# Kernel optimization log

Hardware: AMD Instinct MI355X
Metric: run time of the kernel (lower is better)

## Reference

```python
import jax, jax.numpy as jnp
import numpy as np

N = 1_000_000
LIMS = ((0.0, 51.2), (-25.6, 25.6), (-2.0, 4.4))
SIZES = (256, 256, 32)
GM = np.array([0.2, 0.2, 0.2], np.float32)      # grid_meters
MINS = np.array([0.0, -25.6, -2.0], np.float32)  # xmin, ymin, zmin
OFFSET = 0.5
INIT = 32  # init_size; VFE units = INIT // 2 = 16


def setup_inputs() -> dict:
    key = jax.random.key(0)
    ks = jax.random.split(key, 20)
    lo = jnp.array([l[0] for l in LIMS], jnp.float32)
    hi = jnp.array([l[1] for l in LIMS], jnp.float32)
    # keep points strictly inside lims so quantized idx stays in range
    u = jax.random.uniform(ks[0], (N, 3), minval=1e-3, maxval=1.0 - 1e-3)
    xyz = lo + (hi - lo) * u
    inten = jax.random.uniform(ks[1], (N, 1))
    pc = jnp.concatenate([xyz, inten], axis=1).astype(jnp.float32)
    indicator = jnp.array([0, N // 2, N], jnp.int32)

    def lin(k, o, i):
        return (0.02 * jax.random.normal(k, (o, i), jnp.float32))

    def bias(k, o):
        return (0.02 * jax.random.normal(k, (o,), jnp.float32))

    U = INIT // 2  # 16, VFE units (last_vfe=False)
    return dict(
        pc=pc, indicator=indicator,
        w05=lin(ks[2], U, 10), b05=bias(ks[3], U),
        ww05=lin(ks[4], U, 6), wb05=bias(ks[5], U),
        w1=lin(ks[6], U, 10), b1=bias(ks[7], U),
        ww1=lin(ks[8], U, 6), wb1=bias(ks[9], U),
        am_w=lin(ks[10], INIT, 6), am_b=bias(ks[11], INIT),
        at_w=lin(ks[12], INIT, 2 * INIT), at_b=bias(ks[13], INIT),
        af_w=lin(ks[14], INIT, INIT), af_b=bias(ks[15], INIT),
    )


def _unique_inverse(ids):
    # emulate torch.unique(dim=0, return_inverse=True) via sort+rank on linear voxel ids
    n = ids.shape[0]
    order = jnp.argsort(ids)
    s = ids[order]
    new = jnp.concatenate([jnp.zeros((1,), jnp.int32), (s[1:] != s[:-1]).astype(jnp.int32)])
    ranks = jnp.cumsum(new)
    return jnp.zeros((n,), jnp.int32).at[order].set(ranks)


def _voxel_coords(pc, indicator, scale):
    n = pc.shape[0]
    B = indicator.shape[0] - 1
    bt = jnp.repeat(jnp.arange(B, dtype=jnp.int32), jnp.diff(indicator), total_repeat_length=n)
    nx = int(SIZES[0] // scale); ny = int(SIZES[1] // scale); nz = int(SIZES[2] // scale)
    def quant(col, lim, size):
        idx = (col - lim[0]) / (lim[1] - lim[0]) * float(size)
        return idx.astype(jnp.int32)
    xi = quant(pc[:, 0], LIMS[0], nx)
    yi = quant(pc[:, 1], LIMS[1], ny)
    zi = quant(pc[:, 2], LIMS[2], nz)
    coords = jnp.stack([bt, xi, yi, zi], axis=-1)  # [n,4] bxyz_indx
    lid = ((bt * nx + xi) * ny + yi) * nz + zi     # lexicographic-consistent linear id
    return coords, lid


def _scale_features(pc, coords, inv, Wl, bl, Ww, bw):
    # add_pcmean_and_gridmean + VFELayerMinus (activate=False, gs=None)
    n = pc.shape[0]
    cnt = jax.ops.segment_sum(jnp.ones((n,), jnp.float32), inv, num_segments=n)
    pc_mean = jax.ops.segment_sum(pc[:, :3], inv, num_segments=n) / jnp.maximum(cnt, 1.0)[:, None]
    mm = pc[:, :3] - pc_mean[inv]                                   # pc_mean_minus
    gm = jnp.asarray(GM); mins = jnp.asarray(MINS)
    gmm = pc[:, :3] - ((coords[:, 1:].astype(jnp.float32) + OFFSET) * gm + mins)  # pc_gridmean_minus
    feat = jnp.concatenate([pc, mm, gmm], axis=1)   # [n,10]
    mean = jnp.concatenate([mm, gmm], axis=1)       # [n,6]
    x = feat @ Wl.T + bl                            # [n,16]
    x = x * (mean @ Ww.T + bw)
    mx = jax.ops.segment_max(x, inv, num_segments=n)
    return jnp.concatenate([x, mx[inv]], axis=1), mean  # [n,32], [n,6]


def reference(pc, indicator, w05, b05, ww05, wb05, w1, b1, ww1, wb1,
              am_w, am_b, at_w, at_b, af_w, af_b):
    n = pc.shape[0]
    coords05, lid05 = _voxel_coords(pc, indicator, 0.5)
    coords1, lid1 = _voxel_coords(pc, indicator, 1)
    inv05 = _unique_inverse(lid05)
    inv1 = _unique_inverse(lid1)
    f05, _ = _scale_features(pc, coords05, inv05, w05, b05, ww05, wb05)
    f1, mean1 = _scale_features(pc, coords1, inv1, w1, b1, ww1, wb1)
    agg = jax.nn.relu(mean1 @ am_w.T + am_b) * \
          jax.nn.relu(jnp.concatenate([f05, f1], axis=1) @ at_w.T + at_b)
    agg = agg @ af_w.T + af_b                       # [n,32]
    maxf = jax.ops.segment_max(agg, inv1, num_segments=n)
    cnt = jax.ops.segment_sum(jnp.ones((n,), jnp.float32), inv1, num_segments=n)
    maxf = jnp.where(cnt[:, None] > 0, maxf, 0.0)   # pad empty rows (torch output has no such rows)
    coord_ind = jnp.zeros((n, 4), jnp.int32).at[inv1].set(coords1)  # unique coords, padded to n
    return maxf, coord_ind, inv1
```

## Files before the change

kernel.cpp:

```cpp
#include <hip/hip_runtime.h>
#include <cstdint>
#include <cstdio>


struct Coords { int xi, yi, zi; };

__device__ __forceinline__ Coords quantc(float x, float y, float z, float sx, float sy, float sz) {
    Coords c;
    c.xi = (int)(((x - 0.0f)  / 51.2f) * sx);
    c.yi = (int)(((y + 25.6f) / 51.2f) * sy);
    c.zi = (int)(((z + 2.0f)  / 6.4f)  * sz);
    return c;
}

__device__ __forceinline__ int batch_of(int i, const int* __restrict__ ind, int B) {
    int bt = 0;
    for (int b = 1; b < B; ++b) if (i >= ind[b]) bt = b;
    return bt;
}

__device__ __forceinline__ unsigned f2o(float f) {
    unsigned u = __float_as_uint(f);
    return (u & 0x80000000u) ? ~u : (u | 0x80000000u);
}
__device__ __forceinline__ float o2f(unsigned u) {
    return (u & 0x80000000u) ? __uint_as_float(u ^ 0x80000000u) : __uint_as_float(~u);
}
#define NEG_O 0x007FFFFFu

__device__ __forceinline__ unsigned short f2bf(float x) {
    unsigned u = __float_as_uint(x);
    unsigned r = (u + 0x7FFFu + ((u >> 16) & 1u)) >> 16;
    return (unsigned short)r;
}
__device__ __forceinline__ float bf2f(unsigned h) {
    return __uint_as_float(h << 16);
}

__device__ __forceinline__ void compute_x16(
    float px, float py, float pz, float pw,
    float mx_, float my_, float mz_, Coords c,
    const float* __restrict__ W, const float* __restrict__ Bv,
    const float* __restrict__ Ww, const float* __restrict__ Wb,
    float* __restrict__ x, float* __restrict__ mean6) {
    float gx = px - (((float)c.xi + 0.5f) * 0.2f + 0.0f);
    float gy = py - (((float)c.yi + 0.5f) * 0.2f + (-25.6f));
    float gz = pz - (((float)c.zi + 0.5f) * 0.2f + (-2.0f));
    float mmx = px - mx_, mmy = py - my_, mmz = pz - mz_;
    float feat[10] = {px, py, pz, pw, mmx, mmy, mmz, gx, gy, gz};
    float mean[6]  = {mmx, mmy, mmz, gx, gy, gz};
#pragma unroll
    for (int j = 0; j < 6; ++j) mean6[j] = mean[j];
#pragma unroll
    for (int o = 0; o < 16; ++o) {
        float a = Bv[o];
#pragma unroll
        for (int j = 0; j < 10; ++j) a += feat[j] * W[o * 10 + j];
        float g = Wb[o];
#pragma unroll
        for (int j = 0; j < 6; ++j) g += mean[j] * Ww[o * 6 + j];
        x[o] = a * g;
    }
}


__global__ __launch_bounds__(256) void k_bits(
    const float4* __restrict__ pc, const int* __restrict__ ind, int B, int n,
    unsigned* __restrict__ mask05, unsigned* __restrict__ mask1) {
    int i = blockIdx.x * 256 + threadIdx.x;
    if (i >= n) return;
    float4 p = pc[i];
    int bt = batch_of(i, ind, B);
    Coords c05 = quantc(p.x, p.y, p.z, 512.f, 512.f, 64.f);
    Coords c1  = quantc(p.x, p.y, p.z, 256.f, 256.f, 32.f);
    int lid05 = ((bt * 512 + c05.xi) * 512 + c05.yi) * 64 + c05.zi;
    int lid1  = ((bt * 256 + c1.xi)  * 256 + c1.yi)  * 32 + c1.zi;
    atomicOr(&mask05[lid05 >> 5], 1u << (lid05 & 31));
    atomicOr(&mask1[lid1 >> 5],  1u << (lid1 & 31));
}

__global__ __launch_bounds__(256) void k_chunk2(
    const unsigned* __restrict__ maskA, unsigned* __restrict__ bsumA, int nWA, int nBA,
    const unsigned* __restrict__ maskB, unsigned* __restrict__ bsumB, int nWB) {
    const unsigned* mask; unsigned* bsum; int nW, blk;
    if ((int)blockIdx.x < nBA) { mask = maskA; bsum = bsumA; nW = nWA; blk = blockIdx.x; }
    else { mask = maskB; bsum = bsumB; nW = nWB; blk = blockIdx.x - nBA; }
    int t = threadIdx.x;
    int base = blk * 2048 + t;
    unsigned tot = 0;
#pragma unroll
    for (int k = 0; k < 8; ++k) {
        int w = base + k * 256;
        if (w < nW) tot += __popc(mask[w]);
    }
    __shared__ unsigned s[256];
    s[t] = tot;
    __syncthreads();
    for (int off = 128; off > 0; off >>= 1) {
        if (t < off) s[t] += s[t + off];
        __syncthreads();
    }
    if (t == 0) bsum[blk] = s[0];
}

__global__ __launch_bounds__(256) void k_chunku2(
    const unsigned* __restrict__ cntA, unsigned* __restrict__ bsumA,
    const unsigned* __restrict__ cntB, unsigned* __restrict__ bsumB,
    int nElem, int nCh) {
    const unsigned* val; unsigned* bsum; int blk;
    if ((int)blockIdx.x < nCh) { val = cntA; bsum = bsumA; blk = blockIdx.x; }
    else { val = cntB; bsum = bsumB; blk = blockIdx.x - nCh; }
    int t = threadIdx.x;
    int base = blk * 2048 + t;
    unsigned tot = 0;
#pragma unroll
    for (int k = 0; k < 8; ++k) {
        int w = base + k * 256;
        if (w < nElem) tot += val[w];
    }
    __shared__ unsigned s[256];
    s[t] = tot;
    __syncthreads();
    for (int off = 128; off > 0; off >>= 1) {
        if (t < off) s[t] += s[t + off];
        __syncthreads();
    }
    if (t == 0) bsum[blk] = s[0];
}

__global__ __launch_bounds__(1024) void k_scan2(
    const unsigned* __restrict__ bsumA, unsigned* __restrict__ bprefA,
    unsigned* __restrict__ UoutA, int nA,
    const unsigned* __restrict__ bsumB, unsigned* __restrict__ bprefB,
    unsigned* __restrict__ UoutB, int nB) {
    const unsigned* bsum; unsigned* bpref; unsigned* Uout; int nBn;
    if (blockIdx.x == 0) { bsum = bsumA; bpref = bprefA; Uout = UoutA; nBn = nA; }
    else { bsum = bsumB; bpref = bprefB; Uout = UoutB; nBn = nB; }
    __shared__ unsigned s[1024];
    int t = threadIdx.x;
    int ipt = (nBn + 1023) >> 10;
    unsigned tot = 0;
    for (int k = 0; k < ipt; ++k) {
        int e = t * ipt + k;
        if (e < nBn) tot += bsum[e];
    }
    s[t] = tot;
    __syncthreads();
    for (int off = 1; off < 1024; off <<= 1) {
        unsigned v = 0;
        if (t >= off) v = s[t - off];
        __syncthreads();
        if (t >= off) s[t] += v;
        __syncthreads();
    }
    unsigned run = s[t] - tot;
    for (int k = 0; k < ipt; ++k) {
        int e = t * ipt + k;
        if (e < nBn) { bpref[e] = run; run += bsum[e]; }
    }
    if (t == 1023 && Uout) *Uout = s[1023];
}

__global__ __launch_bounds__(256) void k_wpref2(
    const unsigned* __restrict__ maskA, const unsigned* __restrict__ bprefA,
    unsigned* __restrict__ wprefA, int nWA, int nBA,
    const unsigned* __restrict__ maskB, const unsigned* __restrict__ bprefB,
    unsigned* __restrict__ wprefB, int nWB) {
    const unsigned* mask; const unsigned* bpref; unsigned* wpref; int nW, blk;
    if ((int)blockIdx.x < nBA) { mask = maskA; bpref = bprefA; wpref = wprefA; nW = nWA; blk = blockIdx.x; }
    else { mask = maskB; bpref = bprefB; wpref = wprefB; nW = nWB; blk = blockIdx.x - nBA; }
    int t = threadIdx.x;
    int base = blk * 2048 + t * 8;
    unsigned p[8];
    unsigned tot = 0;
#pragma unroll
    for (int k = 0; k < 8; ++k) {
        int w = base + k;
        p[k] = (w < nW) ? __popc(mask[w]) : 0u;
        tot += p[k];
    }
    __shared__ unsigned s[256];
    s[t] = tot;
    __syncthreads();
    for (int off = 1; off < 256; off <<= 1) {
        unsigned v = 0;
        if (t >= off) v = s[t - off];
        __syncthreads();
        if (t >= off) s[t] += v;
        __syncthreads();
    }
    unsigned run = bpref[blk] + (s[t] - tot);
#pragma unroll
    for (int k = 0; k < 8; ++k) {
        int w = base + k;
        if (w < nW) { wpref[w] = run; run += p[k]; }
    }
}

__global__ __launch_bounds__(256) void k_eprefu2(
    const unsigned* __restrict__ cntA, const unsigned* __restrict__ bprefA,
    unsigned* __restrict__ startA,
    const unsigned* __restrict__ cntB, const unsigned* __restrict__ bprefB,
    unsigned* __restrict__ startB,
    int nElem, int nCh) {
    const unsigned* val; const unsigned* bpref; unsigned* epref; int blk;
    if ((int)blockIdx.x < nCh) { val = cntA; bpref = bprefA; epref = startA; blk = blockIdx.x; }
    else { val = cntB; bpref = bprefB; epref = startB; blk = blockIdx.x - nCh; }
    int t = threadIdx.x;
    int base = blk * 2048 + t * 8;
    unsigned p[8];
    unsigned tot = 0;
#pragma unroll
    for (int k = 0; k < 8; ++k) {
        int w = base + k;
        p[k] = (w < nElem) ? val[w] : 0u;
        tot += p[k];
    }
    __shared__ unsigned s[256];
    s[t] = tot;
    __syncthreads();
    for (int off = 1; off < 256; off <<= 1) {
        unsigned v = 0;
        if (t >= off) v = s[t - off];
        __syncthreads();
        if (t >= off) s[t] += v;
        __syncthreads();
    }
    unsigned run = bpref[blk] + (s[t] - tot);
#pragma unroll
    for (int k = 0; k < 8; ++k) {
        int w = base + k;
        if (w < nElem) { epref[w] = run; run += p[k]; }
    }
}


__global__ __launch_bounds__(256) void k_rank(
    const float4* __restrict__ pc, const int* __restrict__ ind, int B, int n,
    const unsigned* __restrict__ mask05, const unsigned* __restrict__ wp05,
    const unsigned* __restrict__ mask1, const unsigned* __restrict__ wp1,
    unsigned* __restrict__ inv05, unsigned* __restrict__ inv1,
    unsigned* __restrict__ cnt05, unsigned* __restrict__ cnt1,
    unsigned* __restrict__ slot05, unsigned* __restrict__ slot1,
    float* __restrict__ outCoord, float* __restrict__ outInv) {
    int i = blockIdx.x * 256 + threadIdx.x;
    if (i >= n) return;
    float4 p = pc[i];
    int bt = batch_of(i, ind, B);
    Coords c05 = quantc(p.x, p.y, p.z, 512.f, 512.f, 64.f);
    Coords c1  = quantc(p.x, p.y, p.z, 256.f, 256.f, 32.f);
    int lid05 = ((bt * 512 + c05.xi) * 512 + c05.yi) * 64 + c05.zi;
    int lid1  = ((bt * 256 + c1.xi)  * 256 + c1.yi)  * 32 + c1.zi;

    unsigned w = (unsigned)lid05 >> 5, b = (unsigned)lid05 & 31u;
    unsigned r05 = wp05[w] + __popc(mask05[w] & ((1u << b) - 1u));
    w = (unsigned)lid1 >> 5; b = (unsigned)lid1 & 31u;
    unsigned r1 = wp1[w] + __popc(mask1[w] & ((1u << b) - 1u));

    inv05[i] = r05;
    inv1[i] = r1;
    outInv[i] = (float)r1;
    ((float4*)outCoord)[r1] = make_float4((float)bt, (float)c1.xi, (float)c1.yi, (float)c1.zi);

    slot05[i] = atomicAdd(&cnt05[r05], 1u);
    slot1[i]  = atomicAdd(&cnt1[r1], 1u);
}

__global__ __launch_bounds__(256) void k_slot(
    const unsigned* __restrict__ inv05, const unsigned* __restrict__ inv1,
    const unsigned* __restrict__ slot05, const unsigned* __restrict__ slot1,
    const unsigned* __restrict__ start05, const unsigned* __restrict__ start1,
    unsigned* __restrict__ rec05 , unsigned* __restrict__ rec1 , int n) {
    int i = blockIdx.x * 256 + threadIdx.x;
    if (i >= n) return;
    unsigned r05 = inv05[i], r1 = inv1[i];
    unsigned p05 = start05[r05] + slot05[i];
    unsigned p1  = start1[r1] + slot1[i];
    ((uint2*)rec05)[p05] = make_uint2((unsigned)i, r05);
    ((uint4*)rec1)[p1]   = make_uint4((unsigned)i, r1, r05, 0u);
}

__global__ __launch_bounds__(256) void k_segmean2(
    const float4* __restrict__ pc,
    const unsigned* __restrict__ rec05, const unsigned* __restrict__ start05,
    const unsigned* __restrict__ cnt05, float4* __restrict__ mean05,
    const unsigned* __restrict__ rec1, const unsigned* __restrict__ start1,
    const unsigned* __restrict__ cnt1, float4* __restrict__ mean1,
    unsigned char* __restrict__ flags, unsigned* __restrict__ outMaxU,
    int n, int gpts) {
    if ((int)blockIdx.x >= 2 * gpts) {
        int blk3 = blockIdx.x - 2 * gpts;
        int b = blk3 * 256 + threadIdx.x + 1;
        if (b >= gpts) return;
        int j = b * 256;
        if (j >= n) return;
        unsigned r = rec1[(size_t)j * 4 + 1];
        if (start1[r] < (unsigned)j) {
            flags[r] = 1;
            unsigned* row = outMaxU + (size_t)r * 32;
#pragma unroll
            for (int o = 0; o < 32; ++o) row[o] = NEG_O;
        }
        return;
    }
    const unsigned* rec; const unsigned* start; const unsigned* cnt;
    float4* meanOut; int stride, blk;
    if ((int)blockIdx.x < gpts) {
        rec = rec05; start = start05; cnt = cnt05; meanOut = mean05; stride = 2; blk = blockIdx.x;
    } else {
        rec = rec1; start = start1; cnt = cnt1; meanOut = mean1; stride = 4; blk = blockIdx.x - gpts;
    }
    int j = blk * 256 + threadIdx.x;
    int lane = threadIdx.x & 63;
    bool live = j < n;
    unsigned r = 0xFFFFFFFFu;
    float sx = 0.f, sy = 0.f, sz = 0.f;
    if (live) {
        unsigned pi = rec[(size_t)j * stride];
        r = rec[(size_t)j * stride + 1];
        float4 p = pc[pi];
        sx = p.x; sy = p.y; sz = p.z;
    }
#pragma unroll
    for (int d = 1; d < 64; d <<= 1) {
        unsigned rn = (unsigned)__shfl_down((int)r, d);
        float ax = __shfl_down(sx, d);
        float ay = __shfl_down(sy, d);
        float az = __shfl_down(sz, d);
        bool ok = (lane + d) < 64 && rn == r;
        if (ok) { sx += ax; sy += ay; sz += az; }
    }
    if (!live) return;
    if (j != (int)start[r]) return;
    unsigned c = cnt[r];
    unsigned end = j + c;
    unsigned waveEnd = ((unsigned)j & ~63u) + 64u;
    for (unsigned j2 = waveEnd; j2 < end; ++j2) {
        float4 q = pc[rec[(size_t)j2 * stride]];
        sx += q.x; sy += q.y; sz += q.z;
    }
    float cf = (float)c;
    meanOut[r] = make_float4(sx / cf, sy / cf, sz / cf, 0.f);
}

__global__ __launch_bounds__(256) void k_segmx2(
    const float4* __restrict__ pc,
    const unsigned* __restrict__ rec05, const unsigned* __restrict__ start05,
    const unsigned* __restrict__ cnt05, const float4* __restrict__ mean05,
    const float* __restrict__ w05, const float* __restrict__ b05,
    const float* __restrict__ ww05, const float* __restrict__ wb05,
    unsigned short* __restrict__ mx05,
    const unsigned* __restrict__ rec1, const unsigned* __restrict__ start1,
    const unsigned* __restrict__ cnt1, const float4* __restrict__ mean1,
    const float* __restrict__ w1, const float* __restrict__ b1,
    const float* __restrict__ ww1, const float* __restrict__ wb1,
    unsigned short* __restrict__ mx1,
    int n, int gpts) {
    const unsigned* rec; const unsigned* start; const unsigned* cnt;
    const float4* meanIn; const float* W; const float* Bv; const float* Ww;
    const float* Wb; unsigned short* mxOut; int stride, blk;
    float sx_, sy_, sz_;
    if ((int)blockIdx.x < gpts) {
        rec = rec05; start = start05; cnt = cnt05; meanIn = mean05;
        W = w05; Bv = b05; Ww = ww05; Wb = wb05; mxOut = mx05; stride = 2;
        sx_ = 512.f; sy_ = 512.f; sz_ = 64.f; blk = blockIdx.x;
    } else {
        rec = rec1; start = start1; cnt = cnt1; meanIn = mean1;
        W = w1; Bv = b1; Ww = ww1; Wb = wb1; mxOut = mx1; stride = 4;
        sx_ = 256.f; sy_ = 256.f; sz_ = 32.f; blk = blockIdx.x - gpts;
    }
    __shared__ float buf[256][17];
    int t = threadIdx.x;
    int j = blk * 256 + t;
    bool live = j < n;
    unsigned r = 0;
    float x[16], d6[6];
    if (live) {
        unsigned pi = rec[(size_t)j * stride];
        r = rec[(size_t)j * stride + 1];
        float4 p = pc[pi];
        float4 mv = meanIn[r];
        Coords cc = quantc(p.x, p.y, p.z, sx_, sy_, sz_);
        compute_x16(p.x, p.y, p.z, p.w, mv.x, mv.y, mv.z, cc, W, Bv, Ww, Wb, x, d6);
    } else {
#pragma unroll
        for (int o = 0; o < 16; ++o) x[o] = 0.f;
    }
#pragma unroll
    for (int o = 0; o < 16; ++o) buf[t][o] = x[o];
    __syncthreads();
    if (!live || j != (int)start[r]) return;
    unsigned c = cnt[r];
    unsigned end = j + c;
    unsigned blockEnd = ((unsigned)blk + 1u) * 256u;
    unsigned inEnd = end < blockEnd ? end : blockEnd;
    for (unsigned j2 = j + 1; j2 < inEnd; ++j2) {
        int t2 = t + (int)(j2 - (unsigned)j);
#pragma unroll
        for (int o = 0; o < 16; ++o) x[o] = fmaxf(x[o], buf[t2][o]);
    }
    float4 mv = meanIn[r];
    for (unsigned j2 = blockEnd; j2 < end; ++j2) {
        float4 q = pc[rec[(size_t)j2 * stride]];
        Coords cc = quantc(q.x, q.y, q.z, sx_, sy_, sz_);
        float x2[16];
        compute_x16(q.x, q.y, q.z, q.w, mv.x, mv.y, mv.z, cc, W, Bv, Ww, Wb, x2, d6);
#pragma unroll
        for (int o = 0; o < 16; ++o) x[o] = fmaxf(x[o], x2[o]);
    }
    unsigned pk[8];
#pragma unroll
    for (int k = 0; k < 8; ++k)
        pk[k] = (unsigned)f2bf(x[2 * k]) | ((unsigned)f2bf(x[2 * k + 1]) << 16);
    uint4* mr = (uint4*)(mxOut + (size_t)r * 16);
    mr[0] = make_uint4(pk[0], pk[1], pk[2], pk[3]);
    mr[1] = make_uint4(pk[4], pk[5], pk[6], pk[7]);
}

__global__ __launch_bounds__(256, 3) void k_val(
    const float4* __restrict__ pc,
    const unsigned* __restrict__ rec1,
    const unsigned* __restrict__ start1, const unsigned* __restrict__ cnt1,
    const float4* __restrict__ mean05, const unsigned short* __restrict__ mx05,
    const float4* __restrict__ mean1, const unsigned short* __restrict__ mx1,
    const float* __restrict__ w05, const float* __restrict__ b05,
    const float* __restrict__ ww05, const float* __restrict__ wb05,
    const float* __restrict__ w1g, const float* __restrict__ b1g,
    const float* __restrict__ ww1, const float* __restrict__ wb1,
    const float* __restrict__ am_w, const float* __restrict__ am_b,
    const float* __restrict__ at_w, const float* __restrict__ at_b,
    const float* __restrict__ af_w, const float* __restrict__ af_b,
    float* __restrict__ outMax, int n) {
    __shared__ float buf[256][17];
    int t = threadIdx.x;
    int j = blockIdx.x * 256 + t;
    bool live = j < n;
    unsigned r = 0, s = 0, c = 0;
    bool bound = false;
    float at[32];
    if (live) {
        uint4 rc = ((const uint4*)rec1)[j];
        float4 p = pc[rc.x];
        r = rc.y;
        unsigned r05 = rc.z;
        s = start1[r];
        c = cnt1[r];
        bound = (s >> 8) != ((s + c - 1) >> 8);

#pragma unroll
        for (int o = 0; o < 32; ++o) at[o] = at_b[o];

        {
            const uint4* m4 = (const uint4*)(mx1 + (size_t)r * 16);
            uint4 a = m4[0], b2 = m4[1];
            unsigned pw[8] = {a.x, a.y, a.z, a.w, b2.x, b2.y, b2.z, b2.w};
#pragma unroll
            for (int k = 0; k < 8; ++k) {
                float e0 = bf2f(pw[k] & 0xFFFFu);
                float e1 = bf2f(pw[k] >> 16);
#pragma unroll
                for (int o = 0; o < 32; ++o)
                    at[o] += e0 * at_w[o * 64 + 48 + 2 * k] + e1 * at_w[o * 64 + 49 + 2 * k];
            }
        }
        {
            const uint4* m4 = (const uint4*)(mx05 + (size_t)r05 * 16);
            uint4 a = m4[0], b2 = m4[1];
            unsigned pw[8] = {a.x, a.y, a.z, a.w, b2.x, b2.y, b2.z, b2.w};
#pragma unroll
            for (int k = 0; k < 8; ++k) {
                float e0 = bf2f(pw[k] & 0xFFFFu);
                float e1 = bf2f(pw[k] >> 16);
#pragma unroll
                for (int o = 0; o < 32; ++o)
                    at[o] += e0 * at_w[o * 64 + 16 + 2 * k] + e1 * at_w[o * 64 + 17 + 2 * k];
            }
        }
        {
            float4 mv = mean05[r05];
            Coords cc = quantc(p.x, p.y, p.z, 512.f, 512.f, 64.f);
            float gx = p.x - (((float)cc.xi + 0.5f) * 0.1f + 0.0f);
            float gy = p.y - (((float)cc.yi + 0.5f) * 0.1f + (-25.6f));
            float gz = p.z - (((float)cc.zi + 0.5f) * 0.1f + (-2.0f));
            float mmx = p.x - mv.x, mmy = p.y - mv.y, mmz = p.z - mv.z;
            float feat[10] = {p.x, p.y, p.z, p.w, mmx, mmy, mmz, gx, gy, gz};
#pragma unroll
            for (int jj = 0; jj < 16; ++jj) {
                float a_ = b05[jj];
#pragma unroll
                for (int q = 0; q < 10; ++q) a_ += feat[q] * w05[jj * 10 + q];
                float g_ = wb05[jj];
#pragma unroll
                for (int q = 0; q < 6; ++q) g_ += feat[4 + q] * ww05[jj * 6 + q];
                float x_ = a_ * g_;
#pragma unroll
                for (int o = 0; o < 32; ++o) at[o] += x_ * at_w[o * 64 + jj];
            }
        }
        float mean6[6];
        {
            float4 mv = mean1[r];
            Coords cc = quantc(p.x, p.y, p.z, 256.f, 256.f, 32.f);
            float gx = p.x - (((float)cc.xi + 0.5f) * 0.2f + 0.0f);
            float gy = p.y - (((float)cc.yi + 0.5f) * 0.2f + (-25.6f));
            float gz = p.z - (((float)cc.zi + 0.5f) * 0.2f + (-2.0f));
            float mmx = p.x - mv.x, mmy = p.y - mv.y, mmz = p.z - mv.z;
            float feat[10] = {p.x, p.y, p.z, p.w, mmx, mmy, mmz, gx, gy, gz};
            mean6[0] = mmx; mean6[1] = mmy; mean6[2] = mmz;
            mean6[3] = gx;  mean6[4] = gy;  mean6[5] = gz;
#pragma unroll
            for (int jj = 0; jj < 16; ++jj) {
                float a_ = b1g[jj];
#pragma unroll
                for (int q = 0; q < 10; ++q) a_ += feat[q] * w1g[jj * 10 + q];
                float g_ = wb1[jj];
#pragma unroll
                for (int q = 0; q < 6; ++q) g_ += feat[4 + q] * ww1[jj * 6 + q];
                float x_ = a_ * g_;
#pragma unroll
                for (int o = 0; o < 32; ++o) at[o] += x_ * at_w[o * 64 + 32 + jj];
            }
        }
#pragma unroll
        for (int o = 0; o < 32; ++o) {
            float am = am_b[o];
#pragma unroll
            for (int q = 0; q < 6; ++q) am += mean6[q] * am_w[o * 6 + q];
            at[o] = fmaxf(am, 0.f) * fmaxf(at[o], 0.f);
        }
    } else {
#pragma unroll
        for (int o = 0; o < 32; ++o) at[o] = 0.f;
    }

    bool owner = live && !bound && (j == (int)s);
    unsigned end = s + c;
    unsigned* arow = (unsigned*)outMax + (size_t)r * 32;
    float4* ov = (float4*)(outMax + (size_t)r * 32);

    if (live) {
#pragma unroll
        for (int o = 0; o < 16; ++o) {
            float v = af_b[o];
#pragma unroll
            for (int q = 0; q < 32; ++q) v += at[q] * af_w[o * 32 + q];
            if (bound) atomicMax(&arow[o], f2o(v));
            else buf[t][o] = v;
        }
    }
    __syncthreads();
    if (owner) {
        float vm[16];
#pragma unroll
        for (int o = 0; o < 16; ++o) vm[o] = buf[t][o];
        for (unsigned j2 = (unsigned)j + 1; j2 < end; ++j2) {
            int t2 = t + (int)(j2 - (unsigned)j);
#pragma unroll
            for (int o = 0; o < 16; ++o) vm[o] = fmaxf(vm[o], buf[t2][o]);
        }
#pragma unroll
        for (int k = 0; k < 4; ++k)
            ov[k] = make_float4(vm[4 * k], vm[4 * k + 1], vm[4 * k + 2], vm[4 * k + 3]);
    }
    __syncthreads();
    if (live) {
#pragma unroll
        for (int o = 0; o < 16; ++o) {
            float v = af_b[16 + o];
#pragma unroll
            for (int q = 0; q < 32; ++q) v += at[q] * af_w[(16 + o) * 32 + q];
            if (bound) atomicMax(&arow[16 + o], f2o(v));
            else buf[t][o] = v;
        }
    }
    __syncthreads();
    if (owner) {
        float vm[16];
#pragma unroll
        for (int o = 0; o < 16; ++o) vm[o] = buf[t][o];
        for (unsigned j2 = (unsigned)j + 1; j2 < end; ++j2) {
            int t2 = t + (int)(j2 - (unsigned)j);
#pragma unroll
            for (int o = 0; o < 16; ++o) vm[o] = fmaxf(vm[o], buf[t2][o]);
        }
#pragma unroll
        for (int k = 0; k < 4; ++k)
            ov[4 + k] = make_float4(vm[4 * k], vm[4 * k + 1], vm[4 * k + 2], vm[4 * k + 3]);
    }
}

__global__ __launch_bounds__(256) void k_finrow(
    float* __restrict__ outMax, float* __restrict__ outCoord,
    const unsigned char* __restrict__ flags, const unsigned* __restrict__ U1p, int n) {
    int r = blockIdx.x * 256 + threadIdx.x;
    if (r >= n) return;
    unsigned U = *U1p;
    if ((unsigned)r >= U) {
        float4 z = make_float4(0.f, 0.f, 0.f, 0.f);
        float4* row = (float4*)(outMax + (size_t)r * 32);
#pragma unroll
        for (int k = 0; k < 8; ++k) row[k] = z;
        ((float4*)outCoord)[r] = z;
    } else if (flags[r]) {
        unsigned* urow = (unsigned*)outMax + (size_t)r * 32;
        float* frow = outMax + (size_t)r * 32;
#pragma unroll
        for (int o = 0; o < 32; ++o) frow[o] = o2f(urow[o]);
    }
}


extern "C" void kernel_launch(void* const* d_in, const int* in_sizes, int n_in,
                              void* d_out, int out_size, void* d_ws, size_t ws_size,
                              hipStream_t stream) {
    const float4* pc = (const float4*)d_in[0];
    const int* ind   = (const int*)d_in[1];
    const float* w05 = (const float*)d_in[2];
    const float* b05 = (const float*)d_in[3];
    const float* ww05 = (const float*)d_in[4];
    const float* wb05 = (const float*)d_in[5];
    const float* w1  = (const float*)d_in[6];
    const float* b1  = (const float*)d_in[7];
    const float* ww1 = (const float*)d_in[8];
    const float* wb1 = (const float*)d_in[9];
    const float* am_w = (const float*)d_in[10];
    const float* am_b = (const float*)d_in[11];
    const float* at_w = (const float*)d_in[12];
    const float* at_b = (const float*)d_in[13];
    const float* af_w = (const float*)d_in[14];
    const float* af_b = (const float*)d_in[15];

    int n = in_sizes[0] / 4;
    int B = in_sizes[1] - 1;

    int nW05 = B * (512 * 512 * 64 / 32);
    int nW1  = B * (256 * 256 * 32 / 32);
    int nB05 = (nW05 + 2047) / 2048;
    int nB1  = (nW1 + 2047) / 2048;
    int nCh  = (n + 2047) / 2048;

    size_t off = 0;
    char* base = (char*)d_ws;
    auto take = [&](size_t bytes) -> char* {
        char* p = base + off;
        off = (off + bytes + 255) & ~(size_t)255;
        return p;
    };

    unsigned* mask05 = (unsigned*)take((size_t)nW05 * 4);
    unsigned* mask1  = (unsigned*)take((size_t)nW1 * 4);
    unsigned* cnt05  = (unsigned*)take((size_t)n * 4);
    unsigned* cnt1   = (unsigned*)take((size_t)n * 4);
    unsigned char* flags = (unsigned char*)take((size_t)n);
    size_t zeroBytes = off;

    unsigned* wp05   = (unsigned*)take((size_t)nW05 * 4);
    unsigned* wp1    = (unsigned*)take((size_t)nW1 * 4);
    unsigned* inv05  = (unsigned*)take((size_t)n * 4);
    unsigned* inv1   = (unsigned*)take((size_t)n * 4);
    unsigned* slot05 = (unsigned*)take((size_t)n * 4);
    unsigned* slot1  = (unsigned*)take((size_t)n * 4);
    unsigned* start05 = (unsigned*)take((size_t)n * 4);
    unsigned* start1  = (unsigned*)take((size_t)n * 4);
    unsigned* rec05   = (unsigned*)take((size_t)n * 8);
    unsigned* rec1    = (unsigned*)take((size_t)n * 16);
    float4*   mean05  = (float4*)take((size_t)n * 16);
    float4*   mean1   = (float4*)take((size_t)n * 16);
    unsigned short* mx05 = (unsigned short*)take((size_t)n * 32);
    unsigned short* mx1  = (unsigned short*)take((size_t)n * 32);
    unsigned* bsum05  = (unsigned*)take((size_t)nB05 * 4);
    unsigned* bpref05 = (unsigned*)take((size_t)nB05 * 4);
    unsigned* bsum1   = (unsigned*)take((size_t)nB1 * 4);
    unsigned* bpref1  = (unsigned*)take((size_t)nB1 * 4);
    unsigned* bsC05   = (unsigned*)take((size_t)nCh * 4);
    unsigned* bpC05   = (unsigned*)take((size_t)nCh * 4);
    unsigned* bsC1    = (unsigned*)take((size_t)nCh * 4);
    unsigned* bpC1    = (unsigned*)take((size_t)nCh * 4);
    unsigned* U1p     = (unsigned*)take(4);
    size_t total = off;

    if (ws_size < total) {
        fprintf(stderr, "kernel_launch: ws too small (%zu < %zu)\n", ws_size, total);
        return;
    }

    float* outMaxF = (float*)d_out;
    float* outCoord = (float*)d_out + (size_t)n * 32;
    float* outInv = (float*)d_out + (size_t)n * 36;

    hipMemsetAsync(d_ws, 0, zeroBytes, stream);

    int gpts = (n + 255) / 256;
    int nbb  = (gpts + 255) / 256;
    k_bits<<<gpts, 256, 0, stream>>>(pc, ind, B, n, mask05, mask1);
    k_chunk2<<<nB05 + nB1, 256, 0, stream>>>(mask05, bsum05, nW05, nB05,
                                             mask1, bsum1, nW1);
    k_scan2<<<2, 1024, 0, stream>>>(bsum05, bpref05, nullptr, nB05,
                                    bsum1, bpref1, U1p, nB1);
    k_wpref2<<<nB05 + nB1, 256, 0, stream>>>(mask05, bpref05, wp05, nW05, nB05,
                                             mask1, bpref1, wp1, nW1);
    k_rank<<<gpts, 256, 0, stream>>>(pc, ind, B, n, mask05, wp05, mask1, wp1,
                                     inv05, inv1, cnt05, cnt1, slot05, slot1,
                                     outCoord, outInv);
    k_chunku2<<<2 * nCh, 256, 0, stream>>>(cnt05, bsC05, cnt1, bsC1, n, nCh);
    k_scan2<<<2, 1024, 0, stream>>>(bsC05, bpC05, nullptr, nCh,
                                    bsC1, bpC1, nullptr, nCh);
    k_eprefu2<<<2 * nCh, 256, 0, stream>>>(cnt05, bpC05, start05,
                                           cnt1, bpC1, start1, n, nCh);
    k_slot<<<gpts, 256, 0, stream>>>(inv05, inv1, slot05, slot1,
                                     start05, start1, rec05, rec1, n);
    k_segmean2<<<2 * gpts + nbb, 256, 0, stream>>>(pc, rec05, start05, cnt05, mean05,
                                                   rec1, start1, cnt1, mean1,
                                                   flags, (unsigned*)outMaxF, n, gpts);
    k_segmx2<<<2 * gpts, 256, 0, stream>>>(pc,
                                           rec05, start05, cnt05, mean05,
                                           w05, b05, ww05, wb05, mx05,
                                           rec1, start1, cnt1, mean1,
                                           w1, b1, ww1, wb1, mx1, n, gpts);
    k_val<<<gpts, 256, 0, stream>>>(pc, rec1, start1, cnt1,
                                    mean05, mx05, mean1, mx1,
                                    w05, b05, ww05, wb05, w1, b1, ww1, wb1,
                                    am_w, am_b, at_w, at_b, af_w, af_b,
                                    outMaxF, n);
    k_finrow<<<gpts, 256, 0, stream>>>(outMaxF, outCoord, flags, U1p, n);

    (void)n_in; (void)out_size;
}
```

Before: 831.0 us.

## Embed point data in sorted records to avoid indirect point gathers

The slot-scatter kernel now writes each point's xyz and intensity directly into the sorted per-voxel record arrays, along with packed start/count metadata. The downstream mean, max and value kernels read points contiguously instead of gathering pc through an index, and k_val no longer loads start1/cnt1 separately. The rank kernel also writes the output coordinate only from the first point of each voxel instead of every point. The cost is larger records (32 bytes per point per scale) and a scattered 32-byte write in k_slot, plus a count cap at 257 in the packed metadata.

```diff
diff --git a/kernel.cpp b/kernel.cpp
--- a/kernel.cpp
+++ b/kernel.cpp
@@ -260,31 +260,42 @@
     inv05[i] = r05;
     inv1[i] = r1;
     outInv[i] = (float)r1;
-    ((float4*)outCoord)[r1] = make_float4((float)bt, (float)c1.xi, (float)c1.yi, (float)c1.zi);
 
     slot05[i] = atomicAdd(&cnt05[r05], 1u);
-    slot1[i]  = atomicAdd(&cnt1[r1], 1u);
+    unsigned sl1 = atomicAdd(&cnt1[r1], 1u);
+    slot1[i] = sl1;
+    if (sl1 == 0u)
+        ((float4*)outCoord)[r1] = make_float4((float)bt, (float)c1.xi, (float)c1.yi, (float)c1.zi);
 }
 
 __global__ __launch_bounds__(256) void k_slot(
+    const float4* __restrict__ pc,
     const unsigned* __restrict__ inv05, const unsigned* __restrict__ inv1,
     const unsigned* __restrict__ slot05, const unsigned* __restrict__ slot1,
     const unsigned* __restrict__ start05, const unsigned* __restrict__ start1,
-    unsigned* __restrict__ rec05 , unsigned* __restrict__ rec1 , int n) {
+    const unsigned* __restrict__ cnt1,
+    uint4* __restrict__ recA05, uint4* __restrict__ recA1, int n) {
     int i = blockIdx.x * 256 + threadIdx.x;
     if (i >= n) return;
+    float4 p = pc[i];
     unsigned r05 = inv05[i], r1 = inv1[i];
     unsigned p05 = start05[r05] + slot05[i];
-    unsigned p1  = start1[r1] + slot1[i];
-    ((uint2*)rec05)[p05] = make_uint2((unsigned)i, r05);
-    ((uint4*)rec1)[p1]   = make_uint4((unsigned)i, r1, r05, 0u);
+    unsigned s1 = start1[r1];
+    unsigned p1  = s1 + slot1[i];
+    unsigned c1 = cnt1[r1];
+    unsigned cm = c1 < 257u ? c1 : 257u;
+    unsigned meta = s1 | (cm << 23);
+    uint4 pw = *(const uint4*)&p;
+    recA05[(size_t)p05 * 2]     = pw;
+    recA05[(size_t)p05 * 2 + 1] = make_uint4(r05, 0u, 0u, 0u);
+    recA1[(size_t)p1 * 2]       = pw;
+    recA1[(size_t)p1 * 2 + 1]   = make_uint4(r1, r05, meta, 0u);
 }
 
 __global__ __launch_bounds__(256) void k_segmean2(
-    const float4* __restrict__ pc,
-    const unsigned* __restrict__ rec05, const unsigned* __restrict__ start05,
+    const uint4* __restrict__ recA05, const unsigned* __restrict__ start05,
     const unsigned* __restrict__ cnt05, float4* __restrict__ mean05,
-    const unsigned* __restrict__ rec1, const unsigned* __restrict__ start1,
+    const uint4* __restrict__ recA1, const unsigned* __restrict__ start1,
     const unsigned* __restrict__ cnt1, float4* __restrict__ mean1,
     unsigned char* __restrict__ flags, unsigned* __restrict__ outMaxU,
     int n, int gpts) {
@@ -294,7 +305,7 @@
         if (b >= gpts) return;
         int j = b * 256;
         if (j >= n) return;
-        unsigned r = rec1[(size_t)j * 4 + 1];
+        unsigned r = recA1[(size_t)j * 2 + 1].x;
         if (start1[r] < (unsigned)j) {
             flags[r] = 1;
             unsigned* row = outMaxU + (size_t)r * 32;
@@ -303,12 +314,12 @@
         }
         return;
     }
-    const unsigned* rec; const unsigned* start; const unsigned* cnt;
-    float4* meanOut; int stride, blk;
+    const uint4* recA; const unsigned* start; const unsigned* cnt;
+    float4* meanOut; int blk;
     if ((int)blockIdx.x < gpts) {
-        rec = rec05; start = start05; cnt = cnt05; meanOut = mean05; stride = 2; blk = blockIdx.x;
+        recA = recA05; start = start05; cnt = cnt05; meanOut = mean05; blk = blockIdx.x;
     } else {
-        rec = rec1; start = start1; cnt = cnt1; meanOut = mean1; stride = 4; blk = blockIdx.x - gpts;
+        recA = recA1; start = start1; cnt = cnt1; meanOut = mean1; blk = blockIdx.x - gpts;
     }
     int j = blk * 256 + threadIdx.x;
     int lane = threadIdx.x & 63;
@@ -316,9 +327,8 @@
     unsigned r = 0xFFFFFFFFu;
     float sx = 0.f, sy = 0.f, sz = 0.f;
     if (live) {
-        unsigned pi = rec[(size_t)j * stride];
-        r = rec[(size_t)j * stride + 1];
-        float4 p = pc[pi];
+        float4 p = *(const float4*)&recA[(size_t)j * 2];
+        r = recA[(size_t)j * 2 + 1].x;
         sx = p.x; sy = p.y; sz = p.z;
     }
 #pragma unroll
@@ -336,7 +346,7 @@
     unsigned end = j + c;
     unsigned waveEnd = ((unsigned)j & ~63u) + 64u;
     for (unsigned j2 = waveEnd; j2 < end; ++j2) {
-        float4 q = pc[rec[(size_t)j2 * stride]];
+        float4 q = *(const float4*)&recA[(size_t)j2 * 2];
         sx += q.x; sy += q.y; sz += q.z;
     }
     float cf = (float)c;
@@ -344,29 +354,28 @@
 }
 
 __global__ __launch_bounds__(256) void k_segmx2(
-    const float4* __restrict__ pc,
-    const unsigned* __restrict__ rec05, const unsigned* __restrict__ start05,
+    const uint4* __restrict__ recA05, const unsigned* __restrict__ start05,
     const unsigned* __restrict__ cnt05, const float4* __restrict__ mean05,
     const float* __restrict__ w05, const float* __restrict__ b05,
     const float* __restrict__ ww05, const float* __restrict__ wb05,
     unsigned short* __restrict__ mx05,
-    const unsigned* __restrict__ rec1, const unsigned* __restrict__ start1,
+    const uint4* __restrict__ recA1, const unsigned* __restrict__ start1,
     const unsigned* __restrict__ cnt1, const float4* __restrict__ mean1,
     const float* __restrict__ w1, const float* __restrict__ b1,
     const float* __restrict__ ww1, const float* __restrict__ wb1,
     unsigned short* __restrict__ mx1,
     int n, int gpts) {
-    const unsigned* rec; const unsigned* start; const unsigned* cnt;
+    const uint4* recA; const unsigned* start; const unsigned* cnt;
     const float4* meanIn; const float* W; const float* Bv; const float* Ww;
-    const float* Wb; unsigned short* mxOut; int stride, blk;
+    const float* Wb; unsigned short* mxOut; int blk;
     float sx_, sy_, sz_;
     if ((int)blockIdx.x < gpts) {
-        rec = rec05; start = start05; cnt = cnt05; meanIn = mean05;
-        W = w05; Bv = b05; Ww = ww05; Wb = wb05; mxOut = mx05; stride = 2;
+        recA = recA05; start = start05; cnt = cnt05; meanIn = mean05;
+        W = w05; Bv = b05; Ww = ww05; Wb = wb05; mxOut = mx05;
         sx_ = 512.f; sy_ = 512.f; sz_ = 64.f; blk = blockIdx.x;
     } else {
-        rec = rec1; start = start1; cnt = cnt1; meanIn = mean1;
-        W = w1; Bv = b1; Ww = ww1; Wb = wb1; mxOut = mx1; stride = 4;
+        recA = recA1; start = start1; cnt = cnt1; meanIn = mean1;
+        W = w1; Bv = b1; Ww = ww1; Wb = wb1; mxOut = mx1;
         sx_ = 256.f; sy_ = 256.f; sz_ = 32.f; blk = blockIdx.x - gpts;
     }
     __shared__ float buf[256][17];
@@ -376,9 +385,8 @@
     unsigned r = 0;
     float x[16], d6[6];
     if (live) {
-        unsigned pi = rec[(size_t)j * stride];
-        r = rec[(size_t)j * stride + 1];
-        float4 p = pc[pi];
+        float4 p = *(const float4*)&recA[(size_t)j * 2];
+        r = recA[(size_t)j * 2 + 1].x;
         float4 mv = meanIn[r];
         Coords cc = quantc(p.x, p.y, p.z, sx_, sy_, sz_);
         compute_x16(p.x, p.y, p.z, p.w, mv.x, mv.y, mv.z, cc, W, Bv, Ww, Wb, x, d6);
@@ -401,7 +409,7 @@
     }
     float4 mv = meanIn[r];
     for (unsigned j2 = blockEnd; j2 < end; ++j2) {
-        float4 q = pc[rec[(size_t)j2 * stride]];
+        float4 q = *(const float4*)&recA[(size_t)j2 * 2];
         Coords cc = quantc(q.x, q.y, q.z, sx_, sy_, sz_);
         float x2[16];
         compute_x16(q.x, q.y, q.z, q.w, mv.x, mv.y, mv.z, cc, W, Bv, Ww, Wb, x2, d6);
@@ -418,9 +426,7 @@
 }
 
 __global__ __launch_bounds__(256, 3) void k_val(
-    const float4* __restrict__ pc,
-    const unsigned* __restrict__ rec1,
-    const unsigned* __restrict__ start1, const unsigned* __restrict__ cnt1,
+    const uint4* __restrict__ recA1,
     const float4* __restrict__ mean05, const unsigned short* __restrict__ mx05,
     const float4* __restrict__ mean1, const unsigned short* __restrict__ mx1,
     const float* __restrict__ w05, const float* __restrict__ b05,
@@ -439,13 +445,15 @@
     bool bound = false;
     float at[32];
     if (live) {
-        uint4 rc = ((const uint4*)rec1)[j];
-        float4 p = pc[rc.x];
-        r = rc.y;
-        unsigned r05 = rc.z;
-        s = start1[r];
-        c = cnt1[r];
-        bound = (s >> 8) != ((s + c - 1) >> 8);
+        uint4 pw4 = recA1[(size_t)j * 2];
+        float4 p = *(const float4*)&pw4;
+        uint4 mw = recA1[(size_t)j * 2 + 1];
+        r = mw.x;
+        unsigned r05 = mw.y;
+        unsigned meta = mw.z;
+        s = meta & 0x7FFFFFu;
+        c = meta >> 23;
+        bound = (c > 256u) || ((s >> 8) != ((s + c - 1) >> 8));
 
 #pragma unroll
         for (int o = 0; o < 32; ++o) at[o] = at_b[o];
@@ -662,8 +670,8 @@
     unsigned* slot1  = (unsigned*)take((size_t)n * 4);
     unsigned* start05 = (unsigned*)take((size_t)n * 4);
     unsigned* start1  = (unsigned*)take((size_t)n * 4);
-    unsigned* rec05   = (unsigned*)take((size_t)n * 8);
-    unsigned* rec1    = (unsigned*)take((size_t)n * 16);
+    uint4*    recA05  = (uint4*)take((size_t)n * 32);
+    uint4*    recA1   = (uint4*)take((size_t)n * 32);
     float4*   mean05  = (float4*)take((size_t)n * 16);
     float4*   mean1   = (float4*)take((size_t)n * 16);
     unsigned short* mx05 = (unsigned short*)take((size_t)n * 32);
@@ -707,17 +715,16 @@
                                     bsC1, bpC1, nullptr, nCh);
     k_eprefu2<<<2 * nCh, 256, 0, stream>>>(cnt05, bpC05, start05,
                                            cnt1, bpC1, start1, n, nCh);
-    k_slot<<<gpts, 256, 0, stream>>>(inv05, inv1, slot05, slot1,
-                                     start05, start1, rec05, rec1, n);
-    k_segmean2<<<2 * gpts + nbb, 256, 0, stream>>>(pc, rec05, start05, cnt05, mean05,
-                                                   rec1, start1, cnt1, mean1,
+    k_slot<<<gpts, 256, 0, stream>>>(pc, inv05, inv1, slot05, slot1,
+                                     start05, start1, cnt1, recA05, recA1, n);
+    k_segmean2<<<2 * gpts + nbb, 256, 0, stream>>>(recA05, start05, cnt05, mean05,
+                                                   recA1, start1, cnt1, mean1,
                                                    flags, (unsigned*)outMaxF, n, gpts);
-    k_segmx2<<<2 * gpts, 256, 0, stream>>>(pc,
-                                           rec05, start05, cnt05, mean05,
+    k_segmx2<<<2 * gpts, 256, 0, stream>>>(recA05, start05, cnt05, mean05,
                                            w05, b05, ww05, wb05, mx05,
-                                           rec1, start1, cnt1, mean1,
+                                           recA1, start1, cnt1, mean1,
                                            w1, b1, ww1, wb1, mx1, n, gpts);
-    k_val<<<gpts, 256, 0, stream>>>(pc, rec1, start1, cnt1,
+    k_val<<<gpts, 256, 0, stream>>>(recA1,
                                     mean05, mx05, mean1, mx1,
                                     w05, b05, ww05, wb05, w1, b1, ww1, wb1,
                                     am_w, am_b, at_w, at_b, af_w, af_b,
```

Measured after the change: 827.6 us. No clear change (-0.4%).
